# Performance work log

Measured on AMD Instinct MI355X. Metric: run time of the kernel, lower is better.

Reference implementation:

```python
import jax, jax.numpy as jnp
import numpy as np

B, S, V, D, H = 8, 256, 32000, 1024, 1024
NLAY_H, NLAY_L, HEADS = 2, 2, 8
RATIO, N_LOW, N_HIGH = 4, 16, 4
HD = H // HEADS


def setup_inputs():
    key = jax.random.key(0)
    ks = jax.random.split(key, 16)
    s = 0.02
    f = lambda k, shape: (jax.random.normal(k, shape) * s).astype(jnp.float32)
    return {
        "input_ids": jax.random.randint(ks[0], (B, S), 0, V),
        "emb": f(ks[1], (V, D)),
        "pos": f(ks[2], (S, D)),
        "Wih_h": f(ks[3], (NLAY_H, 3 * H, H)),
        "bih_h": jnp.zeros((NLAY_H, 3 * H), jnp.float32),
        "Whh_h": f(ks[4], (NLAY_H, 3 * H, H)),
        "bhh_h": jnp.zeros((NLAY_H, 3 * H), jnp.float32),
        "Win": f(ks[5], (H, 2 * H)),
        "bin_": jnp.zeros((H,), jnp.float32),
        "Wq": f(ks[6], (H, H)),
        "Wk": f(ks[7], (H, H)),
        "Wv": f(ks[8], (H, H)),
        "Wo": f(ks[9], (H, H)),
        "Wih_l": f(ks[10], (NLAY_L, 3 * H, H)),
        "bih_l": jnp.zeros((NLAY_L, 3 * H), jnp.float32),
        "Whh_l": f(ks[11], (NLAY_L, 3 * H, H)),
        "bhh_l": jnp.zeros((NLAY_L, 3 * H), jnp.float32),
        "ln_g": jnp.ones((H,), jnp.float32),
        "ln_b": jnp.zeros((H,), jnp.float32),
        "Wout": f(ks[12], (V, H)),
    }


def gru_cell(x, h, Wih, bih, Whh, bhh):
    gx = x @ Wih.T + bih  # [B, 3H]
    gh = h @ Whh.T + bhh
    xr, xz, xn = jnp.split(gx, 3, axis=-1)
    hr, hz, hn = jnp.split(gh, 3, axis=-1)
    r = jax.nn.sigmoid(xr + hr)
    z = jax.nn.sigmoid(xz + hz)
    n = jnp.tanh(xn + r * hn)
    return (1.0 - z) * n + z * h


def _forward(input_ids, emb, pos, Wih_h, bih_h, Whh_h, bhh_h, Win, bin_,
             Wq, Wk, Wv, Wo, Wih_l, bih_l, Whh_l, bhh_l, ln_g, ln_b, Wout):
    embeds = emb[input_ids] + pos[None, :S]  # [B, S, D]
    inv_sqrt_hd = np.float32(1.0 / np.sqrt(HD))

    def high_mod(x, hs):  # hs: [NLAY_H, B, H]
        new = []
        for l in range(NLAY_H):
            x = gru_cell(x, hs[l], Wih_h[l], bih_h[l], Whh_h[l], bhh_h[l])
            new.append(x)
        return jnp.stack(new), x

    def low_mod(x, high_cur, hist, mask, ls):
        # input projection over [embed ; current high state]
        inp = jax.nn.gelu(jnp.concatenate([x, high_cur], axis=-1) @ Win.T + bin_)  # [B, H]
        # multi-head cross-attention over high-state history (causal in high steps)
        q = (inp @ Wq.T).reshape(B, HEADS, HD)
        k = (hist @ Wk.T).reshape(B, N_HIGH, HEADS, HD)
        v = (hist @ Wv.T).reshape(B, N_HIGH, HEADS, HD)
        scores = jnp.einsum('bhd,bthd->bht', q, k) * inv_sqrt_hd
        scores = jnp.where(mask[None, None, :], scores, jnp.float32(-1e9))
        attn = jax.nn.softmax(scores, axis=-1)
        ctx = jnp.einsum('bht,bthd->bhd', attn, v).reshape(B, H) @ Wo.T
        x2 = inp + ctx
        new = []
        for l in range(NLAY_L):
            x2 = gru_cell(x2, ls[l], Wih_l[l], bih_l[l], Whh_l[l], bhh_l[l])
            new.append(x2)
        return jnp.stack(new), x2

    def step(carry, t):
        hs_all, ls_all, hist = carry
        e = embeds[:, t]  # [B, D]
        low_step = t % N_LOW
        high_step = low_step // RATIO
        do_high = (low_step % RATIO) == 0
        hs = hs_all[high_step]
        new_hs, high_out = high_mod(e, hs)
        hs_all = hs_all.at[high_step].set(jnp.where(do_high, new_hs, hs))
        hist = hist.at[:, high_step].set(jnp.where(do_high, high_out, hist[:, high_step]))
        mask = jnp.arange(N_HIGH) <= high_step
        ls = ls_all[low_step]
        new_ls, low_out = low_mod(e, hist[:, high_step], hist, mask, ls)
        ls_all = ls_all.at[low_step].set(new_ls)
        mu = low_out.mean(axis=-1, keepdims=True)
        var = ((low_out - mu) ** 2).mean(axis=-1, keepdims=True)
        y = (low_out - mu) / jnp.sqrt(var + 1e-5) * ln_g + ln_b
        return (hs_all, ls_all, hist), y @ Wout.T  # [B, V]

    hs0 = jnp.zeros((N_HIGH, NLAY_H, B, H), jnp.float32)
    ls0 = jnp.zeros((N_LOW, NLAY_L, B, H), jnp.float32)
    hist0 = jnp.zeros((B, N_HIGH, H), jnp.float32)
    _, logits = jax.lax.scan(step, (hs0, ls0, hist0), jnp.arange(S))
    return jnp.transpose(logits, (1, 0, 2))  # [B, S, V]


def reference(input_ids, emb, pos, Wih_h, bih_h, Whh_h, bhh_h, Win, bin_,
              Wq, Wk, Wv, Wo, Wih_l, bih_l, Whh_l, bhh_l, ln_g, ln_b, Wout):
    return _forward(input_ids, emb, pos, Wih_h, bih_h, Whh_h, bhh_h, Win, bin_,
                    Wq, Wk, Wv, Wo, Wih_l, bih_l, Whh_l, bhh_l, ln_g, ln_b, Wout)
```

## Files before the change

kernel.cpp:

```cpp
#include <hip/hip_runtime.h>

typedef unsigned short u16;
typedef float f32x4 __attribute__((ext_vector_type(4)));
typedef __bf16 bf16x8 __attribute__((ext_vector_type(8)));
typedef u16 u16x8 __attribute__((ext_vector_type(8)));

#define DEVFN __device__ __forceinline__


DEVFN u16 f2bf(float f) {
  unsigned u = __builtin_bit_cast(unsigned, f);
  unsigned r = u + 0x7FFFu + ((u >> 16) & 1u);
  return (u16)(r >> 16);
}

DEVFN bf16x8 cvt8(const float* p) {
  float4 f0 = *reinterpret_cast<const float4*>(p);
  float4 f1 = *reinterpret_cast<const float4*>(p + 4);
  u16x8 u;
  u[0] = f2bf(f0.x); u[1] = f2bf(f0.y); u[2] = f2bf(f0.z); u[3] = f2bf(f0.w);
  u[4] = f2bf(f1.x); u[5] = f2bf(f1.y); u[6] = f2bf(f1.z); u[7] = f2bf(f1.w);
  return __builtin_bit_cast(bf16x8, u);
}

DEVFN bf16x8 ldbf(const u16* p) { return *reinterpret_cast<const bf16x8*>(p); }
DEVFN float sigm(float x) { return 1.f / (1.f + expf(-x)); }

DEVFN void gload16(const u16* g, u16* l) {
  __builtin_amdgcn_global_load_lds(
      (const __attribute__((address_space(1))) void*)g,
      (__attribute__((address_space(3))) void*)l, 16, 0, 0);
}

template<int NTSTORE, int OUTF, int BF16OUT, int CADD>
__global__ __launch_bounds__(256) void gemm_lds(
    const u16* __restrict__ A, const u16* __restrict__ W,
    const float* __restrict__ Cadd,
    float* __restrict__ OUT, u16* __restrict__ OUTbf,
    int ldo, int mtiles) {
  __shared__ u16 smA[2][128 * 32];
  __shared__ u16 smB[2][128 * 32];

  int nwg = gridDim.x;
  int orig = blockIdx.x;
  int q = nwg >> 3, r = nwg & 7;
  int xcd = orig & 7, idx = orig >> 3;
  int wg = (xcd < r ? xcd * (q + 1) : r * (q + 1) + (xcd - r) * q) + idx;
  int m0 = (wg % mtiles) * 128;
  int n0 = (wg / mtiles) * 128;

  int tid = threadIdx.x;
  int wv = tid >> 6, lane = tid & 63;
  int lrow = lane >> 2;
  int gcol = ((lane & 3) ^ ((lrow >> 1) & 3)) << 3;

  const u16* gA = A + (size_t)(m0 + wv * 32 + lrow) * 1024 + gcol;
  const u16* gB = W + (size_t)(n0 + wv * 32 + lrow) * 1024 + gcol;
  u16* lA0 = &smA[0][(wv * 32) * 32];
  u16* lA1 = &smA[0][(wv * 32 + 16) * 32];
  u16* lB0 = &smB[0][(wv * 32) * 32];
  u16* lB1 = &smB[0][(wv * 32 + 16) * 32];
  const int BUFO = 128 * 32;

  f32x4 acc[4][4];
#pragma unroll
  for (int mi = 0; mi < 4; ++mi)
#pragma unroll
    for (int ni = 0; ni < 4; ++ni) acc[mi][ni] = f32x4{0.f, 0.f, 0.f, 0.f};

  int qm = (wv >> 1) * 64, qn = (wv & 1) * 64;
  int lr = lane & 15;
  int kk = (lane >> 4) << 3;

  int offA[4], offB[4];
#pragma unroll
  for (int i = 0; i < 4; ++i) {
    int ra = qm + i * 16 + lr;
    offA[i] = ra * 64 + ((kk ^ (((ra >> 1) & 3) << 3)) << 1);
    int rbw = qn + i * 16 + lr;
    offB[i] = rbw * 64 + ((kk ^ (((rbw >> 1) & 3) << 3)) << 1);
  }
  const char* baseA = (const char*)&smA[0][0];
  const char* baseB = (const char*)&smB[0][0];

  gload16(gA, lA0);
  gload16(gA + 16 * 1024, lA1);
  gload16(gB, lB0);
  gload16(gB + 16 * 1024, lB1);

  for (int kt = 0; kt < 32; ++kt) {
    int buf = kt & 1;
    __syncthreads();
    if (kt < 31) {
      int k0 = (kt + 1) << 5;
      int bo = (buf ^ 1) * BUFO;
      gload16(gA + k0, lA0 + bo);
      gload16(gA + 16 * 1024 + k0, lA1 + bo);
      gload16(gB + k0, lB0 + bo);
      gload16(gB + 16 * 1024 + k0, lB1 + bo);
    }
    int bb = buf * (BUFO * 2);
    bf16x8 av[4], bv[4];
#pragma unroll
    for (int i = 0; i < 4; ++i) {
      av[i] = *(const bf16x8*)(baseA + bb + offA[i]);
      bv[i] = *(const bf16x8*)(baseB + bb + offB[i]);
    }
#pragma unroll
    for (int mi = 0; mi < 4; ++mi)
#pragma unroll
      for (int ni = 0; ni < 4; ++ni)
        acc[mi][ni] = __builtin_amdgcn_mfma_f32_16x16x32_bf16(av[mi], bv[ni], acc[mi][ni], 0, 0, 0);
  }

  int rb = (lane >> 4) << 2;
#pragma unroll
  for (int mi = 0; mi < 4; ++mi)
#pragma unroll
    for (int ni = 0; ni < 4; ++ni)
#pragma unroll
      for (int rr = 0; rr < 4; ++rr) {
        int row = m0 + qm + mi * 16 + rb + rr;
        int col = n0 + qn + ni * 16 + lr;
        size_t o = (size_t)row * (size_t)ldo + col;
        float v = acc[mi][ni][rr];
        if constexpr (CADD) v += Cadd[o];
        if constexpr (OUTF) {
          if constexpr (NTSTORE) __builtin_nontemporal_store(v, &OUT[o]);
          else OUT[o] = v;
        }
        if constexpr (BF16OUT) OUTbf[o] = f2bf(v);
      }
}

template<int MT, int NT, int KW>
__global__ __launch_bounds__(64 * KW) void gemm2(
    const u16* __restrict__ A, int lda,
    const void* __restrict__ Wp, int ldw, int kwoff, int wbf,
    const float* __restrict__ Cadd, int ldc,
    float* __restrict__ OUT, u16* __restrict__ OUTbf, int ldo, int K) {
  int tid = threadIdx.x;
  int kw = tid >> 6;
  int lane = tid & 63;
  int lr = lane & 15;
  int kk = (lane >> 4) << 3;
  int n0 = blockIdx.x * (16 * NT);
  int m0 = blockIdx.y * (16 * MT);
  int KP = K / KW;
  int kb = kw * KP + kk;

  f32x4 acc[MT][NT];
#pragma unroll
  for (int mi = 0; mi < MT; ++mi)
#pragma unroll
    for (int ni = 0; ni < NT; ++ni) acc[mi][ni] = f32x4{0.f, 0.f, 0.f, 0.f};

  const u16* ap[MT];
#pragma unroll
  for (int mi = 0; mi < MT; ++mi) ap[mi] = A + (size_t)(m0 + mi * 16 + lr) * (size_t)lda + kb;

  if (wbf) {
    const u16* wb[NT];
#pragma unroll
    for (int ni = 0; ni < NT; ++ni)
      wb[ni] = (const u16*)Wp + (size_t)(n0 + ni * 16 + lr) * (size_t)ldw + kwoff + kb;
    for (int k0 = 0; k0 < KP; k0 += 32) {
      bf16x8 wv[NT];
#pragma unroll
      for (int ni = 0; ni < NT; ++ni) wv[ni] = ldbf(wb[ni] + k0);
#pragma unroll
      for (int mi = 0; mi < MT; ++mi) {
        bf16x8 a = ldbf(ap[mi] + k0);
#pragma unroll
        for (int ni = 0; ni < NT; ++ni)
          acc[mi][ni] = __builtin_amdgcn_mfma_f32_16x16x32_bf16(a, wv[ni], acc[mi][ni], 0, 0, 0);
      }
    }
  } else {
    const float* wf[NT];
#pragma unroll
    for (int ni = 0; ni < NT; ++ni)
      wf[ni] = (const float*)Wp + (size_t)(n0 + ni * 16 + lr) * (size_t)ldw + kwoff + kb;
    for (int k0 = 0; k0 < KP; k0 += 32) {
      bf16x8 wv[NT];
#pragma unroll
      for (int ni = 0; ni < NT; ++ni) wv[ni] = cvt8(wf[ni] + k0);
#pragma unroll
      for (int mi = 0; mi < MT; ++mi) {
        bf16x8 a = ldbf(ap[mi] + k0);
#pragma unroll
        for (int ni = 0; ni < NT; ++ni)
          acc[mi][ni] = __builtin_amdgcn_mfma_f32_16x16x32_bf16(a, wv[ni], acc[mi][ni], 0, 0, 0);
      }
    }
  }

  if constexpr (KW > 1) {
    __shared__ f32x4 red[KW][MT * NT][64];
#pragma unroll
    for (int mi = 0; mi < MT; ++mi)
#pragma unroll
      for (int ni = 0; ni < NT; ++ni) red[kw][mi * NT + ni][lane] = acc[mi][ni];
    __syncthreads();
    if (kw) return;
    for (int w2 = 1; w2 < KW; ++w2)
#pragma unroll
      for (int mi = 0; mi < MT; ++mi)
#pragma unroll
        for (int ni = 0; ni < NT; ++ni) acc[mi][ni] += red[w2][mi * NT + ni][lane];
  }

  int rb = (lane >> 4) << 2;
#pragma unroll
  for (int mi = 0; mi < MT; ++mi)
#pragma unroll
    for (int ni = 0; ni < NT; ++ni)
#pragma unroll
      for (int rr = 0; rr < 4; ++rr) {
        int row = m0 + mi * 16 + rb + rr;
        int col = n0 + ni * 16 + lr;
        size_t o = (size_t)row * (size_t)ldo + col;
        float v = acc[mi][ni][rr];
        if (Cadd) v += Cadd[(size_t)row * (size_t)ldc + col];
        if (OUT) OUT[o] = v;
        if (OUTbf) OUTbf[o] = f2bf(v);
      }
}

struct GruP {
  const u16* X; const u16* Hb; const float* Hf;
  const u16* Wbih; const u16* Wbhh;
  const float* Wfih; const float* Wfhh;
  const float* bih; const float* bhh;
  float* Hof; u16* Hob; u16* hist;
};

__global__ __launch_bounds__(256) void gru_dual(GruP pa, GruP pb, int tiles1, int wbf) {
  GruP p; int m0;
  if ((int)blockIdx.y < tiles1) { p = pa; m0 = blockIdx.y * 32; }
  else { p = pb; m0 = ((int)blockIdx.y - tiles1) * 32; }
  int tid = threadIdx.x;
  int kw = tid >> 6;
  int lane = tid & 63;
  int lr = lane & 15;
  int kk = (lane >> 4) << 3;
  int j0 = blockIdx.x * 16;
  const int KP = 256;
  int kb = kw * KP + kk;

  f32x4 aR[2], aZ[2], aNX[2], aNH[2];
#pragma unroll
  for (int mi = 0; mi < 2; ++mi) {
    aR[mi] = f32x4{0.f, 0.f, 0.f, 0.f};
    aZ[mi] = f32x4{0.f, 0.f, 0.f, 0.f};
    aNX[mi] = f32x4{0.f, 0.f, 0.f, 0.f};
    aNH[mi] = f32x4{0.f, 0.f, 0.f, 0.f};
  }

  const u16* xp[2];
  const u16* hp[2];
#pragma unroll
  for (int mi = 0; mi < 2; ++mi) {
    size_t ro = (size_t)(m0 + mi * 16 + lr) * 1024 + kb;
    xp[mi] = p.X + ro;
    hp[mi] = p.Hb + ro;
  }

  size_t wro = (size_t)(j0 + lr) * 1024 + kb;
  if (wbf) {
    const u16 *pxr = p.Wbih + wro, *pxz = p.Wbih + wro + 1048576, *pxn = p.Wbih + wro + 2097152;
    const u16 *phr = p.Wbhh + wro, *phz = p.Wbhh + wro + 1048576, *phn = p.Wbhh + wro + 2097152;
    for (int k0 = 0; k0 < KP; k0 += 32) {
      bf16x8 wxr = ldbf(pxr + k0), wxz = ldbf(pxz + k0), wxn = ldbf(pxn + k0);
      bf16x8 whr = ldbf(phr + k0), whz = ldbf(phz + k0), whn = ldbf(phn + k0);
#pragma unroll
      for (int mi = 0; mi < 2; ++mi) {
        bf16x8 ax = ldbf(xp[mi] + k0);
        bf16x8 ah = ldbf(hp[mi] + k0);
        aR[mi] = __builtin_amdgcn_mfma_f32_16x16x32_bf16(ax, wxr, aR[mi], 0, 0, 0);
        aR[mi] = __builtin_amdgcn_mfma_f32_16x16x32_bf16(ah, whr, aR[mi], 0, 0, 0);
        aZ[mi] = __builtin_amdgcn_mfma_f32_16x16x32_bf16(ax, wxz, aZ[mi], 0, 0, 0);
        aZ[mi] = __builtin_amdgcn_mfma_f32_16x16x32_bf16(ah, whz, aZ[mi], 0, 0, 0);
        aNX[mi] = __builtin_amdgcn_mfma_f32_16x16x32_bf16(ax, wxn, aNX[mi], 0, 0, 0);
        aNH[mi] = __builtin_amdgcn_mfma_f32_16x16x32_bf16(ah, whn, aNH[mi], 0, 0, 0);
      }
    }
  } else {
    const float *pxr = p.Wfih + wro, *pxz = p.Wfih + wro + 1048576, *pxn = p.Wfih + wro + 2097152;
    const float *phr = p.Wfhh + wro, *phz = p.Wfhh + wro + 1048576, *phn = p.Wfhh + wro + 2097152;
    for (int k0 = 0; k0 < KP; k0 += 32) {
      bf16x8 wxr = cvt8(pxr + k0), wxz = cvt8(pxz + k0), wxn = cvt8(pxn + k0);
      bf16x8 whr = cvt8(phr + k0), whz = cvt8(phz + k0), whn = cvt8(phn + k0);
#pragma unroll
      for (int mi = 0; mi < 2; ++mi) {
        bf16x8 ax = ldbf(xp[mi] + k0);
        bf16x8 ah = ldbf(hp[mi] + k0);
        aR[mi] = __builtin_amdgcn_mfma_f32_16x16x32_bf16(ax, wxr, aR[mi], 0, 0, 0);
        aR[mi] = __builtin_amdgcn_mfma_f32_16x16x32_bf16(ah, whr, aR[mi], 0, 0, 0);
        aZ[mi] = __builtin_amdgcn_mfma_f32_16x16x32_bf16(ax, wxz, aZ[mi], 0, 0, 0);
        aZ[mi] = __builtin_amdgcn_mfma_f32_16x16x32_bf16(ah, whz, aZ[mi], 0, 0, 0);
        aNX[mi] = __builtin_amdgcn_mfma_f32_16x16x32_bf16(ax, wxn, aNX[mi], 0, 0, 0);
        aNH[mi] = __builtin_amdgcn_mfma_f32_16x16x32_bf16(ah, whn, aNH[mi], 0, 0, 0);
      }
    }
  }

  {
    __shared__ f32x4 red[4][8][64];
#pragma unroll
    for (int mi = 0; mi < 2; ++mi) {
      red[kw][mi * 4 + 0][lane] = aR[mi];
      red[kw][mi * 4 + 1][lane] = aZ[mi];
      red[kw][mi * 4 + 2][lane] = aNX[mi];
      red[kw][mi * 4 + 3][lane] = aNH[mi];
    }
    __syncthreads();
    if (kw) return;
    for (int w2 = 1; w2 < 4; ++w2)
#pragma unroll
      for (int mi = 0; mi < 2; ++mi) {
        aR[mi] += red[w2][mi * 4 + 0][lane];
        aZ[mi] += red[w2][mi * 4 + 1][lane];
        aNX[mi] += red[w2][mi * 4 + 2][lane];
        aNH[mi] += red[w2][mi * 4 + 3][lane];
      }
  }

  int c = j0 + lr;
  float br = p.bih[c] + p.bhh[c];
  float bz = p.bih[1024 + c] + p.bhh[1024 + c];
  float bnx = p.bih[2048 + c];
  float bnh = p.bhh[2048 + c];
  int rb = (lane >> 4) << 2;
#pragma unroll
  for (int mi = 0; mi < 2; ++mi)
#pragma unroll
    for (int rr = 0; rr < 4; ++rr) {
      int row = m0 + mi * 16 + rb + rr;
      float r = sigm(aR[mi][rr] + br);
      float z = sigm(aZ[mi][rr] + bz);
      float n = tanhf(aNX[mi][rr] + bnx + r * (aNH[mi][rr] + bnh));
      size_t o = (size_t)row * 1024 + c;
      float hv = (1.f - z) * n + z * p.Hf[o];
      p.Hof[o] = hv;
      u16 hb = f2bf(hv);
      p.Hob[o] = hb;
      if (p.hist) p.hist[o] = hb;
    }
}

__global__ __launch_bounds__(256) void gemm_big(const u16* __restrict__ A,
                                                const void* __restrict__ Wp, int wbf,
                                                float* __restrict__ OUT) {
  int wv = threadIdx.x >> 6;
  int lane = threadIdx.x & 63;
  int lr = lane & 15;
  int kk = (lane >> 4) << 3;
  int m0 = blockIdx.x * 256 + wv * 64;
  int n0 = blockIdx.y * 64;

  f32x4 acc[4][4];
#pragma unroll
  for (int mi = 0; mi < 4; ++mi)
#pragma unroll
    for (int ni = 0; ni < 4; ++ni) acc[mi][ni] = f32x4{0.f, 0.f, 0.f, 0.f};

  const u16* ap[4];
#pragma unroll
  for (int mi = 0; mi < 4; ++mi) ap[mi] = A + (size_t)(m0 + mi * 16 + lr) * 1024 + kk;

  const float* wf[4];
#pragma unroll
  for (int ni = 0; ni < 4; ++ni) wf[ni] = (const float*)Wp + (size_t)(n0 + ni * 16 + lr) * 1024 + kk;
  for (int k0 = 0; k0 < 1024; k0 += 32) {
    bf16x8 wvv[4];
#pragma unroll
    for (int ni = 0; ni < 4; ++ni) wvv[ni] = cvt8(wf[ni] + k0);
#pragma unroll
    for (int mi = 0; mi < 4; ++mi) {
      bf16x8 a = ldbf(ap[mi] + k0);
#pragma unroll
      for (int ni = 0; ni < 4; ++ni)
        acc[mi][ni] = __builtin_amdgcn_mfma_f32_16x16x32_bf16(a, wvv[ni], acc[mi][ni], 0, 0, 0);
    }
  }

  int rb = (lane >> 4) << 2;
#pragma unroll
  for (int mi = 0; mi < 4; ++mi)
#pragma unroll
    for (int ni = 0; ni < 4; ++ni)
#pragma unroll
      for (int rr = 0; rr < 4; ++rr) {
        size_t o = (size_t)(m0 + mi * 16 + rb + rr) * 32000 + (size_t)(n0 + ni * 16 + lr);
        __builtin_nontemporal_store(acc[mi][ni][rr], &OUT[o]);
      }
}

struct CvtSeg { const float* src; u16* dst; int src_ld; int col_off; int log2c; int nblk; };
struct CvtArgs { CvtSeg seg[11]; int nseg; };

__global__ void cvt_all(CvtArgs a) {
  int blk = blockIdx.x;
  int s = 0;
  while (s < a.nseg - 1 && blk >= a.seg[s].nblk) { blk -= a.seg[s].nblk; ++s; }
  const CvtSeg g = a.seg[s];
  size_t idx = ((size_t)blk * 256 + threadIdx.x) * 8;
  size_t row = idx >> g.log2c;
  int col = (int)(idx & ((1u << g.log2c) - 1));
  const float* sp = g.src + row * (size_t)g.src_ld + g.col_off + col;
  *reinterpret_cast<u16x8*>(g.dst + idx) = __builtin_bit_cast(u16x8, cvt8(sp));
}

__global__ void embed_kernel(const int* __restrict__ ids, const float* __restrict__ emb,
                             const float* __restrict__ pos, u16* __restrict__ out) {
  int idx = blockIdx.x * 256 + threadIdx.x;
  int e8 = (idx & 127) << 3;
  int rb = idx >> 7;
  int t = rb >> 3, b = rb & 7;
  int w = t >> 4, lsp = t & 15, g = lsp >> 2, o = lsp & 3;
  int R = ((w << 4) + (o << 2) + g) * 8 + b;
  int tok = ids[b * 256 + t];
  const float* ep = emb + (size_t)tok * 1024 + e8;
  const float* pp = pos + (size_t)t * 1024 + e8;
  u16x8 u;
#pragma unroll
  for (int i = 0; i < 8; ++i) u[i] = f2bf(ep[i] + pp[i]);
  *reinterpret_cast<u16x8*>(out + (size_t)R * 1024 + e8) = u;
}

__global__ void inp_all(const float* __restrict__ einp, const float* __restrict__ kvhAll,
                        const float* __restrict__ bin, float* __restrict__ inpb,
                        u16* __restrict__ inpbf) {
  int idx = blockIdx.x * 256 + threadIdx.x;
  int r = idx >> 10, j = idx & 1023;
  int w = r >> 7, r7 = r & 127;
  int g = (r7 >> 3) & 3, b = r7 & 7;
  float x = einp[idx] + kvhAll[(size_t)(w * 32 + g * 8 + b) * 3072 + 2048 + j] + bin[j];
  float t = tanhf(0.7978845608028654f * (x + 0.044715f * x * x * x));
  float v = 0.5f * x * (1.f + t);
  inpb[idx] = v;
  inpbf[idx] = f2bf(v);
}

__global__ void attn_all(const float* __restrict__ qb, const float* __restrict__ kvhAll,
                         u16* __restrict__ ctxbf) {
  int r = blockIdx.x;
  int w = r >> 7, r7 = r & 127;
  int sp = r7 >> 3;
  int g = sp & 3;
  int b = r7 & 7;
  int lane = threadIdx.x;
  const float* kvb = kvhAll + (size_t)w * 32 * 3072;
  __shared__ float aw[8][4];
  if (lane < 32) {
    int head = lane >> 2, t = lane & 3;
    float s = 0.f;
    if (t <= g) {
      const float* qp = qb + (size_t)r * 1024 + head * 128;
      const float* kp = kvb + (size_t)(t * 8 + b) * 3072 + head * 128;
      for (int d = 0; d < 128; ++d) s += qp[d] * kp[d];
      s *= 0.08838834764831845f;
    }
    float sc[4];
    sc[0] = __shfl(s, (head << 2) + 0);
    sc[1] = __shfl(s, (head << 2) + 1);
    sc[2] = __shfl(s, (head << 2) + 2);
    sc[3] = __shfl(s, (head << 2) + 3);
    if (t == 0) {
      float mx = -1e30f;
      for (int u = 0; u <= g; ++u) mx = fmaxf(mx, sc[u]);
      float p[4] = {0.f, 0.f, 0.f, 0.f};
      float den = 0.f;
      for (int u = 0; u <= g; ++u) { p[u] = expf(sc[u] - mx); den += p[u]; }
      float inv = 1.f / den;
      for (int u = 0; u < 4; ++u) aw[head][u] = (u <= g) ? p[u] * inv : 0.f;
    }
  }
  __syncthreads();
  for (int idx = lane; idx < 1024; idx += 64) {
    int head = idx >> 7;
    float acc = 0.f;
#pragma unroll
    for (int t = 0; t < 4; ++t) acc += aw[head][t] * kvb[(size_t)(t * 8 + b) * 3072 + 1024 + idx];
    ctxbf[(size_t)r * 1024 + idx] = f2bf(acc);
  }
}

__global__ void ln_all(const float* __restrict__ ls1f, const float* __restrict__ g_,
                       const float* __restrict__ b_, u16* __restrict__ Ybf) {
  int bid = blockIdx.x;
  int w = bid >> 7, r7 = bid & 127;
  int tid = threadIdx.x;
  const float* x = ls1f + (size_t)(w + 1) * 131072 + (size_t)r7 * 1024;
  float s = 0.f, s2 = 0.f;
  for (int j = tid; j < 1024; j += 256) { float v = x[j]; s += v; s2 += v * v; }
  for (int off = 32; off; off >>= 1) { s += __shfl_xor(s, off); s2 += __shfl_xor(s2, off); }
  __shared__ float rs[4], rs2[4], mv[2];
  int wv = tid >> 6;
  if ((tid & 63) == 0) { rs[wv] = s; rs2[wv] = s2; }
  __syncthreads();
  if (tid == 0) {
    float S = rs[0] + rs[1] + rs[2] + rs[3];
    float S2 = rs2[0] + rs2[1] + rs2[2] + rs2[3];
    float mu = S * (1.f / 1024.f);
    float var = S2 * (1.f / 1024.f) - mu * mu;
    mv[0] = mu;
    mv[1] = rsqrtf(var + 1e-5f);
  }
  __syncthreads();
  float mu = mv[0], rstd = mv[1];
  int sp = r7 >> 3, b = r7 & 7;
  int g = sp & 3, o = sp >> 2;
  int t = w * 16 + g * 4 + o;
  u16* yrow = Ybf + (size_t)(b * 256 + t) * 1024;
  for (int j = tid; j < 1024; j += 256) {
    float v = (x[j] - mu) * rstd * g_[j] + b_[j];
    yrow[j] = f2bf(v);
  }
}

extern "C" void kernel_launch(void* const* d_in, const int* in_sizes, int n_in,
                              void* d_out, int out_size, void* d_ws, size_t ws_size,
                              hipStream_t stream) {
  const int* ids = (const int*)d_in[0];
  const float* emb = (const float*)d_in[1];
  const float* pos = (const float*)d_in[2];
  const float* Wih_h = (const float*)d_in[3];
  const float* bih_h = (const float*)d_in[4];
  const float* Whh_h = (const float*)d_in[5];
  const float* bhh_h = (const float*)d_in[6];
  const float* Win = (const float*)d_in[7];
  const float* bin_ = (const float*)d_in[8];
  const float* Wq = (const float*)d_in[9];
  const float* Wk = (const float*)d_in[10];
  const float* Wv = (const float*)d_in[11];
  const float* Wo = (const float*)d_in[12];
  const float* Wih_l = (const float*)d_in[13];
  const float* bih_l = (const float*)d_in[14];
  const float* Whh_l = (const float*)d_in[15];
  const float* bhh_l = (const float*)d_in[16];
  const float* ln_g = (const float*)d_in[17];
  const float* ln_b = (const float*)d_in[18];
  const float* Wout = (const float*)d_in[19];
  float* out = (float*)d_out;

  size_t off = 0;
  char* wsb = (char*)d_ws;
  auto allocF = [&](size_t n) { float* p = (float*)(wsb + off); off += n * 4; return p; };
  auto allocU = [&](size_t n) { u16* p = (u16*)(wsb + off); off += n * 2; return p; };

  float* hs0f = allocF((size_t)17 * 32768);
  float* hs1f = allocF((size_t)17 * 32768);
  float* ls0f = allocF((size_t)17 * 131072);
  float* ls1f = allocF((size_t)17 * 131072);
  u16* hs0b = allocU((size_t)17 * 32768);
  u16* hs1b = allocU((size_t)17 * 32768);
  u16* ls0b = allocU((size_t)17 * 131072);
  u16* ls1b = allocU((size_t)17 * 131072);
  u16* histAll = allocU(524288);
  u16* embB = allocU(2097152);
  float* einp = allocF(2097152);
  float* kvhAll = allocF((size_t)512 * 3072);
  float* inpb = allocF(2097152);
  u16* inpbf = allocU(2097152);
  float* qb = allocF(2097152);
  u16* ctxbf = allocU(2097152);
  u16* x2bf = allocU(2097152);
  u16* Ybf = allocU(2097152);

  const size_t WPACK_BYTES = (size_t)(4 * 6291456 + 1048576 + 1048576 + 1048576 + 3145728) * 2;
  bool packW = (off + WPACK_BYTES <= ws_size);
  u16 *WihHb = nullptr, *WhhHb = nullptr, *WihLb = nullptr, *WhhLb = nullptr;
  u16 *WinB0 = nullptr, *WqB = nullptr, *WoB = nullptr, *KVp = nullptr;
  if (packW) {
    WihHb = allocU(6291456);
    WhhHb = allocU(6291456);
    WihLb = allocU(6291456);
    WhhLb = allocU(6291456);
    WinB0 = allocU(1048576);
    WqB = allocU(1048576);
    WoB = allocU(1048576);
    KVp = allocU(3145728);
  }
  bool packWout = packW && (off + (size_t)32768000 * 2 <= ws_size);
  u16* WoutB = nullptr;
  if (packWout) WoutB = allocU(32768000);

  (void)hipMemsetAsync(hs0f, 0, 32768 * 4, stream);
  (void)hipMemsetAsync(hs1f, 0, 32768 * 4, stream);
  (void)hipMemsetAsync(ls0f, 0, 131072 * 4, stream);
  (void)hipMemsetAsync(ls1f, 0, 131072 * 4, stream);
  (void)hipMemsetAsync(hs0b, 0, 32768 * 2, stream);
  (void)hipMemsetAsync(hs1b, 0, 32768 * 2, stream);
  (void)hipMemsetAsync(ls0b, 0, 131072 * 2, stream);
  (void)hipMemsetAsync(ls1b, 0, 131072 * 2, stream);

  embed_kernel<<<1024, 256, 0, stream>>>(ids, emb, pos, embB);
  if (packW) {
    CvtArgs ca{};
    int ns = 0, tot = 0;
    auto add = [&](const float* s, u16* d, int ld, int co, int l2c, size_t nelem) {
      int nb = (int)(nelem / 2048);
      ca.seg[ns++] = CvtSeg{s, d, ld, co, l2c, nb};
      tot += nb;
    };
    add(Wih_h, WihHb, 1024, 0, 10, 6291456);
    add(Whh_h, WhhHb, 1024, 0, 10, 6291456);
    add(Wih_l, WihLb, 1024, 0, 10, 6291456);
    add(Whh_l, WhhLb, 1024, 0, 10, 6291456);
    add(Win, WinB0, 2048, 0, 10, 1048576);
    add(Wq, WqB, 1024, 0, 10, 1048576);
    add(Wo, WoB, 1024, 0, 10, 1048576);
    add(Wk, KVp, 1024, 0, 10, 1048576);
    add(Wv, KVp + 1048576, 1024, 0, 10, 1048576);
    add(Win, KVp + 2097152, 2048, 1024, 10, 1048576);
    if (packWout) add(Wout, WoutB, 1024, 0, 10, 32768000);
    ca.nseg = ns;
    cvt_all<<<tot, 256, 0, stream>>>(ca);
  }
  int wbfW = packW ? 1 : 0;

  if (packW)
    gemm_lds<0, 1, 0, 0><<<128, 256, 0, stream>>>(embB, WinB0, nullptr, einp, nullptr, 1024, 16);
  else
    gemm2<2, 2, 2><<<dim3(32, 64), 128, 0, stream>>>(
        embB, 1024, Win, 2048, 0, 0, nullptr, 0, einp, nullptr, 1024, 1024);

  const size_t LW = (size_t)3072 * 1024;
  auto HP = [&](int layer, int w) {
    GruP p;
    if (layer == 0) {
      p.X = embB + (size_t)w * 131072;
      p.Hb = hs0b + (size_t)w * 32768; p.Hf = hs0f + (size_t)w * 32768;
      p.Wbih = WihHb; p.Wbhh = WhhHb; p.Wfih = Wih_h; p.Wfhh = Whh_h;
      p.bih = bih_h; p.bhh = bhh_h;
      p.Hof = hs0f + (size_t)(w + 1) * 32768; p.Hob = hs0b + (size_t)(w + 1) * 32768;
      p.hist = nullptr;
    } else {
      p.X = hs0b + (size_t)(w + 1) * 32768;
      p.Hb = hs1b + (size_t)w * 32768; p.Hf = hs1f + (size_t)w * 32768;
      p.Wbih = WihHb ? WihHb + LW : nullptr; p.Wbhh = WhhHb ? WhhHb + LW : nullptr;
      p.Wfih = Wih_h + LW; p.Wfhh = Whh_h + LW;
      p.bih = bih_h + 3072; p.bhh = bhh_h + 3072;
      p.Hof = hs1f + (size_t)(w + 1) * 32768; p.Hob = hs1b + (size_t)(w + 1) * 32768;
      p.hist = histAll + (size_t)w * 32768;
    }
    return p;
  };
  auto LP = [&](int layer, int w) {
    GruP p;
    if (layer == 0) {
      p.X = x2bf + (size_t)w * 131072;
      p.Hb = ls0b + (size_t)w * 131072; p.Hf = ls0f + (size_t)w * 131072;
      p.Wbih = WihLb; p.Wbhh = WhhLb; p.Wfih = Wih_l; p.Wfhh = Whh_l;
      p.bih = bih_l; p.bhh = bhh_l;
      p.Hof = ls0f + (size_t)(w + 1) * 131072; p.Hob = ls0b + (size_t)(w + 1) * 131072;
      p.hist = nullptr;
    } else {
      p.X = ls0b + (size_t)(w + 1) * 131072;
      p.Hb = ls1b + (size_t)w * 131072; p.Hf = ls1f + (size_t)w * 131072;
      p.Wbih = WihLb ? WihLb + LW : nullptr; p.Wbhh = WhhLb ? WhhLb + LW : nullptr;
      p.Wfih = Wih_l + LW; p.Wfhh = Whh_l + LW;
      p.bih = bih_l + 3072; p.bhh = bhh_l + 3072;
      p.Hof = ls1f + (size_t)(w + 1) * 131072; p.Hob = ls1b + (size_t)(w + 1) * 131072;
      p.hist = nullptr;
    }
    return p;
  };

  gru_dual<<<dim3(64, 1), 256, 0, stream>>>(HP(0, 0), HP(0, 0), 1, wbfW);
  for (int d = 1; d <= 15; ++d)
    gru_dual<<<dim3(64, 2), 256, 0, stream>>>(HP(1, d - 1), HP(0, d), 1, wbfW);
  gru_dual<<<dim3(64, 1), 256, 0, stream>>>(HP(1, 15), HP(1, 15), 1, wbfW);

  if (packW) {
    gemm_lds<0, 1, 0, 0><<<96, 256, 0, stream>>>(histAll, KVp, nullptr, kvhAll, nullptr, 3072, 4);
  } else {
    gemm2<2, 2, 2><<<dim3(32, 16), 128, 0, stream>>>(
        histAll, 1024, Wk, 1024, 0, 0, nullptr, 0, kvhAll, nullptr, 3072, 1024);
    gemm2<2, 2, 2><<<dim3(32, 16), 128, 0, stream>>>(
        histAll, 1024, Wv, 1024, 0, 0, nullptr, 0, kvhAll + 1024, nullptr, 3072, 1024);
    gemm2<2, 2, 2><<<dim3(32, 16), 128, 0, stream>>>(
        histAll, 1024, Win, 2048, 1024, 0, nullptr, 0, kvhAll + 2048, nullptr, 3072, 1024);
  }
  inp_all<<<8192, 256, 0, stream>>>(einp, kvhAll, bin_, inpb, inpbf);
  if (packW)
    gemm_lds<0, 1, 0, 0><<<128, 256, 0, stream>>>(inpbf, WqB, nullptr, qb, nullptr, 1024, 16);
  else
    gemm2<2, 2, 2><<<dim3(32, 64), 128, 0, stream>>>(
        inpbf, 1024, Wq, 1024, 0, 0, nullptr, 0, qb, nullptr, 1024, 1024);
  attn_all<<<2048, 64, 0, stream>>>(qb, kvhAll, ctxbf);
  if (packW)
    gemm_lds<0, 0, 1, 1><<<128, 256, 0, stream>>>(ctxbf, WoB, inpb, nullptr, x2bf, 1024, 16);
  else
    gemm2<2, 2, 2><<<dim3(32, 64), 128, 0, stream>>>(
        ctxbf, 1024, Wo, 1024, 0, 0, inpb, 1024, nullptr, x2bf, 1024, 1024);

  gru_dual<<<dim3(64, 4), 256, 0, stream>>>(LP(0, 0), LP(0, 0), 4, wbfW);
  for (int d = 1; d <= 15; ++d)
    gru_dual<<<dim3(64, 8), 256, 0, stream>>>(LP(1, d - 1), LP(0, d), 4, wbfW);
  gru_dual<<<dim3(64, 4), 256, 0, stream>>>(LP(1, 15), LP(1, 15), 4, wbfW);

  ln_all<<<2048, 256, 0, stream>>>(ls1f, ln_g, ln_b, Ybf);
  if (packWout)
    gemm_lds<1, 1, 0, 0><<<4000, 256, 0, stream>>>(Ybf, WoutB, nullptr, out, nullptr, 32000, 16);
  else
    gemm_big<<<dim3(8, 500), 256, 0, stream>>>(Ybf, Wout, 0, out);
}
```

Before: 1.081 ms.

## Replace per-step GRU kernel launches with persistent cooperative grid-synced kernel

Replaces the 17 separate gru_dual launches for each wavefront-pipelined GRU chain (high and low modules) with a single cooperative kernel that loops over the diagonal steps and uses grid.sync between them. The goal is to remove kernel launch and inter-launch gaps on the sequential critical path. In exchange it adds grid-wide barrier costs, and idle blocks must still join every barrier. It falls back to the launch loop if the cooperative launch fails, and the GRU body is factored into a shared device function.

```diff
diff --git a/kernel.cpp b/kernel.cpp
--- a/kernel.cpp
+++ b/kernel.cpp
@@ -1,4 +1,7 @@
 #include <hip/hip_runtime.h>
+#include <hip/hip_cooperative_groups.h>
+
+namespace cg = cooperative_groups;
 
 typedef unsigned short u16;
 typedef float f32x4 __attribute__((ext_vector_type(4)));
@@ -227,6 +230,140 @@
       }
 }
 
+DEVFN void gru_step_body(const u16* __restrict__ X, const u16* __restrict__ Hb,
+                         const float* __restrict__ Hf,
+                         const u16* __restrict__ Wih, const u16* __restrict__ Whh,
+                         const float* __restrict__ bih, const float* __restrict__ bhh,
+                         float* __restrict__ Hof, u16* __restrict__ Hob,
+                         u16* __restrict__ hist,
+                         int m0, int j0, int kw, int lane,
+                         f32x4 (*red)[8][64]) {
+  int lr = lane & 15;
+  int kk = (lane >> 4) << 3;
+  const int KP = 256;
+  int kb = kw * KP + kk;
+
+  f32x4 aR[2], aZ[2], aNX[2], aNH[2];
+#pragma unroll
+  for (int mi = 0; mi < 2; ++mi) {
+    aR[mi] = f32x4{0.f, 0.f, 0.f, 0.f};
+    aZ[mi] = f32x4{0.f, 0.f, 0.f, 0.f};
+    aNX[mi] = f32x4{0.f, 0.f, 0.f, 0.f};
+    aNH[mi] = f32x4{0.f, 0.f, 0.f, 0.f};
+  }
+
+  const u16* xp[2];
+  const u16* hp[2];
+#pragma unroll
+  for (int mi = 0; mi < 2; ++mi) {
+    size_t ro = (size_t)(m0 + mi * 16 + lr) * 1024 + kb;
+    xp[mi] = X + ro;
+    hp[mi] = Hb + ro;
+  }
+
+  size_t wro = (size_t)(j0 + lr) * 1024 + kb;
+  const u16 *pxr = Wih + wro, *pxz = Wih + wro + 1048576, *pxn = Wih + wro + 2097152;
+  const u16 *phr = Whh + wro, *phz = Whh + wro + 1048576, *phn = Whh + wro + 2097152;
+  for (int k0 = 0; k0 < KP; k0 += 32) {
+    bf16x8 wxr = ldbf(pxr + k0), wxz = ldbf(pxz + k0), wxn = ldbf(pxn + k0);
+    bf16x8 whr = ldbf(phr + k0), whz = ldbf(phz + k0), whn = ldbf(phn + k0);
+#pragma unroll
+    for (int mi = 0; mi < 2; ++mi) {
+      bf16x8 ax = ldbf(xp[mi] + k0);
+      bf16x8 ah = ldbf(hp[mi] + k0);
+      aR[mi] = __builtin_amdgcn_mfma_f32_16x16x32_bf16(ax, wxr, aR[mi], 0, 0, 0);
+      aR[mi] = __builtin_amdgcn_mfma_f32_16x16x32_bf16(ah, whr, aR[mi], 0, 0, 0);
+      aZ[mi] = __builtin_amdgcn_mfma_f32_16x16x32_bf16(ax, wxz, aZ[mi], 0, 0, 0);
+      aZ[mi] = __builtin_amdgcn_mfma_f32_16x16x32_bf16(ah, whz, aZ[mi], 0, 0, 0);
+      aNX[mi] = __builtin_amdgcn_mfma_f32_16x16x32_bf16(ax, wxn, aNX[mi], 0, 0, 0);
+      aNH[mi] = __builtin_amdgcn_mfma_f32_16x16x32_bf16(ah, whn, aNH[mi], 0, 0, 0);
+    }
+  }
+
+#pragma unroll
+  for (int mi = 0; mi < 2; ++mi) {
+    red[kw][mi * 4 + 0][lane] = aR[mi];
+    red[kw][mi * 4 + 1][lane] = aZ[mi];
+    red[kw][mi * 4 + 2][lane] = aNX[mi];
+    red[kw][mi * 4 + 3][lane] = aNH[mi];
+  }
+  __syncthreads();
+  if (kw == 0) {
+    for (int w2 = 1; w2 < 4; ++w2)
+#pragma unroll
+      for (int mi = 0; mi < 2; ++mi) {
+        aR[mi] += red[w2][mi * 4 + 0][lane];
+        aZ[mi] += red[w2][mi * 4 + 1][lane];
+        aNX[mi] += red[w2][mi * 4 + 2][lane];
+        aNH[mi] += red[w2][mi * 4 + 3][lane];
+      }
+    int c = j0 + lr;
+    float br = bih[c] + bhh[c];
+    float bz = bih[1024 + c] + bhh[1024 + c];
+    float bnx = bih[2048 + c];
+    float bnh = bhh[2048 + c];
+    int rb = (lane >> 4) << 2;
+#pragma unroll
+    for (int mi = 0; mi < 2; ++mi)
+#pragma unroll
+      for (int rr = 0; rr < 4; ++rr) {
+        int row = m0 + mi * 16 + rb + rr;
+        float r = sigm(aR[mi][rr] + br);
+        float z = sigm(aZ[mi][rr] + bz);
+        float n = tanhf(aNX[mi][rr] + bnx + r * (aNH[mi][rr] + bnh));
+        size_t o = (size_t)row * 1024 + c;
+        float hv = (1.f - z) * n + z * Hf[o];
+        Hof[o] = hv;
+        u16 hb = f2bf(hv);
+        Hob[o] = hb;
+        if (hist) hist[o] = hb;
+      }
+  }
+}
+
+struct ChainArgs {
+  const u16* X0; size_t xstride;
+  float* h0f; u16* h0b;
+  float* h1f; u16* h1b;
+  size_t sstride;
+  const u16* Wih; const u16* Whh;
+  const float* bih; const float* bhh;
+  u16* hist;
+  int nm;
+};
+
+__global__ __launch_bounds__(256) void gru_chain(ChainArgs A) {
+  cg::grid_group grid = cg::this_grid();
+  __shared__ f32x4 red[4][8][64];
+  int tid = threadIdx.x;
+  int kw = tid >> 6, lane = tid & 63;
+  int j0 = blockIdx.x * 16;
+  int yy = blockIdx.y;
+  int probA = (yy < A.nm) ? 1 : 0;
+  int m0 = (probA ? yy : yy - A.nm) * 32;
+  const size_t LW = (size_t)3072 * 1024;
+
+  for (int d = 0; d <= 16; ++d) {
+    int active = probA ? (d >= 1) : (d <= 15);
+    if (active) {
+      int w = probA ? d - 1 : d;
+      int layer = probA;
+      const u16* X = probA ? (A.h0b + (size_t)(w + 1) * A.sstride)
+                           : (A.X0 + (size_t)w * A.xstride);
+      float* hf = layer ? A.h1f : A.h0f;
+      u16* hb = layer ? A.h1b : A.h0b;
+      gru_step_body(X, hb + (size_t)w * A.sstride, hf + (size_t)w * A.sstride,
+                    A.Wih + (size_t)layer * LW, A.Whh + (size_t)layer * LW,
+                    A.bih + layer * 3072, A.bhh + layer * 3072,
+                    hf + (size_t)(w + 1) * A.sstride, hb + (size_t)(w + 1) * A.sstride,
+                    (probA && A.hist) ? (A.hist + (size_t)w * 32768) : nullptr,
+                    m0, j0, kw, lane, red);
+    }
+    __threadfence();
+    grid.sync();
+  }
+}
+
 struct GruP {
   const u16* X; const u16* Hb; const float* Hf;
   const u16* Wbih; const u16* Wbhh;
@@ -247,6 +384,13 @@
   int j0 = blockIdx.x * 16;
   const int KP = 256;
   int kb = kw * KP + kk;
+  __shared__ f32x4 red[4][8][64];
+
+  if (wbf) {
+    gru_step_body(p.X, p.Hb, p.Hf, p.Wbih, p.Wbhh, p.bih, p.bhh,
+                  p.Hof, p.Hob, p.hist, m0, j0, kw, lane, red);
+    return;
+  }
 
   f32x4 aR[2], aZ[2], aNX[2], aNH[2];
 #pragma unroll
@@ -256,7 +400,6 @@
     aNX[mi] = f32x4{0.f, 0.f, 0.f, 0.f};
     aNH[mi] = f32x4{0.f, 0.f, 0.f, 0.f};
   }
-
   const u16* xp[2];
   const u16* hp[2];
 #pragma unroll
@@ -265,67 +408,41 @@
     xp[mi] = p.X + ro;
     hp[mi] = p.Hb + ro;
   }
-
   size_t wro = (size_t)(j0 + lr) * 1024 + kb;
-  if (wbf) {
-    const u16 *pxr = p.Wbih + wro, *pxz = p.Wbih + wro + 1048576, *pxn = p.Wbih + wro + 2097152;
-    const u16 *phr = p.Wbhh + wro, *phz = p.Wbhh + wro + 1048576, *phn = p.Wbhh + wro + 2097152;
-    for (int k0 = 0; k0 < KP; k0 += 32) {
-      bf16x8 wxr = ldbf(pxr + k0), wxz = ldbf(pxz + k0), wxn = ldbf(pxn + k0);
-      bf16x8 whr = ldbf(phr + k0), whz = ldbf(phz + k0), whn = ldbf(phn + k0);
-#pragma unroll
-      for (int mi = 0; mi < 2; ++mi) {
-        bf16x8 ax = ldbf(xp[mi] + k0);
-        bf16x8 ah = ldbf(hp[mi] + k0);
-        aR[mi] = __builtin_amdgcn_mfma_f32_16x16x32_bf16(ax, wxr, aR[mi], 0, 0, 0);
-        aR[mi] = __builtin_amdgcn_mfma_f32_16x16x32_bf16(ah, whr, aR[mi], 0, 0, 0);
-        aZ[mi] = __builtin_amdgcn_mfma_f32_16x16x32_bf16(ax, wxz, aZ[mi], 0, 0, 0);
-        aZ[mi] = __builtin_amdgcn_mfma_f32_16x16x32_bf16(ah, whz, aZ[mi], 0, 0, 0);
-        aNX[mi] = __builtin_amdgcn_mfma_f32_16x16x32_bf16(ax, wxn, aNX[mi], 0, 0, 0);
-        aNH[mi] = __builtin_amdgcn_mfma_f32_16x16x32_bf16(ah, whn, aNH[mi], 0, 0, 0);
-      }
-    }
-  } else {
-    const float *pxr = p.Wfih + wro, *pxz = p.Wfih + wro + 1048576, *pxn = p.Wfih + wro + 2097152;
-    const float *phr = p.Wfhh + wro, *phz = p.Wfhh + wro + 1048576, *phn = p.Wfhh + wro + 2097152;
-    for (int k0 = 0; k0 < KP; k0 += 32) {
-      bf16x8 wxr = cvt8(pxr + k0), wxz = cvt8(pxz + k0), wxn = cvt8(pxn + k0);
-      bf16x8 whr = cvt8(phr + k0), whz = cvt8(phz + k0), whn = cvt8(phn + k0);
-#pragma unroll
-      for (int mi = 0; mi < 2; ++mi) {
-        bf16x8 ax = ldbf(xp[mi] + k0);
-        bf16x8 ah = ldbf(hp[mi] + k0);
-        aR[mi] = __builtin_amdgcn_mfma_f32_16x16x32_bf16(ax, wxr, aR[mi], 0, 0, 0);
-        aR[mi] = __builtin_amdgcn_mfma_f32_16x16x32_bf16(ah, whr, aR[mi], 0, 0, 0);
-        aZ[mi] = __builtin_amdgcn_mfma_f32_16x16x32_bf16(ax, wxz, aZ[mi], 0, 0, 0);
-        aZ[mi] = __builtin_amdgcn_mfma_f32_16x16x32_bf16(ah, whz, aZ[mi], 0, 0, 0);
-        aNX[mi] = __builtin_amdgcn_mfma_f32_16x16x32_bf16(ax, wxn, aNX[mi], 0, 0, 0);
-        aNH[mi] = __builtin_amdgcn_mfma_f32_16x16x32_bf16(ah, whn, aNH[mi], 0, 0, 0);
-      }
-    }
-  }
-
-  {
-    __shared__ f32x4 red[4][8][64];
+  const float *pxr = p.Wfih + wro, *pxz = p.Wfih + wro + 1048576, *pxn = p.Wfih + wro + 2097152;
+  const float *phr = p.Wfhh + wro, *phz = p.Wfhh + wro + 1048576, *phn = p.Wfhh + wro + 2097152;
+  for (int k0 = 0; k0 < KP; k0 += 32) {
+    bf16x8 wxr = cvt8(pxr + k0), wxz = cvt8(pxz + k0), wxn = cvt8(pxn + k0);
+    bf16x8 whr = cvt8(phr + k0), whz = cvt8(phz + k0), whn = cvt8(phn + k0);
 #pragma unroll
     for (int mi = 0; mi < 2; ++mi) {
-      red[kw][mi * 4 + 0][lane] = aR[mi];
-      red[kw][mi * 4 + 1][lane] = aZ[mi];
-      red[kw][mi * 4 + 2][lane] = aNX[mi];
-      red[kw][mi * 4 + 3][lane] = aNH[mi];
-    }
-    __syncthreads();
-    if (kw) return;
-    for (int w2 = 1; w2 < 4; ++w2)
-#pragma unroll
-      for (int mi = 0; mi < 2; ++mi) {
-        aR[mi] += red[w2][mi * 4 + 0][lane];
-        aZ[mi] += red[w2][mi * 4 + 1][lane];
-        aNX[mi] += red[w2][mi * 4 + 2][lane];
-        aNH[mi] += red[w2][mi * 4 + 3][lane];
-      }
-  }
-
+      bf16x8 ax = ldbf(xp[mi] + k0);
+      bf16x8 ah = ldbf(hp[mi] + k0);
+      aR[mi] = __builtin_amdgcn_mfma_f32_16x16x32_bf16(ax, wxr, aR[mi], 0, 0, 0);
+      aR[mi] = __builtin_amdgcn_mfma_f32_16x16x32_bf16(ah, whr, aR[mi], 0, 0, 0);
+      aZ[mi] = __builtin_amdgcn_mfma_f32_16x16x32_bf16(ax, wxz, aZ[mi], 0, 0, 0);
+      aZ[mi] = __builtin_amdgcn_mfma_f32_16x16x32_bf16(ah, whz, aZ[mi], 0, 0, 0);
+      aNX[mi] = __builtin_amdgcn_mfma_f32_16x16x32_bf16(ax, wxn, aNX[mi], 0, 0, 0);
+      aNH[mi] = __builtin_amdgcn_mfma_f32_16x16x32_bf16(ah, whn, aNH[mi], 0, 0, 0);
+    }
+  }
+#pragma unroll
+  for (int mi = 0; mi < 2; ++mi) {
+    red[kw][mi * 4 + 0][lane] = aR[mi];
+    red[kw][mi * 4 + 1][lane] = aZ[mi];
+    red[kw][mi * 4 + 2][lane] = aNX[mi];
+    red[kw][mi * 4 + 3][lane] = aNH[mi];
+  }
+  __syncthreads();
+  if (kw) return;
+  for (int w2 = 1; w2 < 4; ++w2)
+#pragma unroll
+    for (int mi = 0; mi < 2; ++mi) {
+      aR[mi] += red[w2][mi * 4 + 0][lane];
+      aZ[mi] += red[w2][mi * 4 + 1][lane];
+      aNX[mi] += red[w2][mi * 4 + 2][lane];
+      aNH[mi] += red[w2][mi * 4 + 3][lane];
+    }
   int c = j0 + lr;
   float br = p.bih[c] + p.bhh[c];
   float bz = p.bih[1024 + c] + p.bhh[1024 + c];
@@ -668,11 +785,33 @@
     }
     return p;
   };
-
-  gru_dual<<<dim3(64, 1), 256, 0, stream>>>(HP(0, 0), HP(0, 0), 1, wbfW);
-  for (int d = 1; d <= 15; ++d)
-    gru_dual<<<dim3(64, 2), 256, 0, stream>>>(HP(1, d - 1), HP(0, d), 1, wbfW);
-  gru_dual<<<dim3(64, 1), 256, 0, stream>>>(HP(1, 15), HP(1, 15), 1, wbfW);
+  auto high_loop = [&]() {
+    gru_dual<<<dim3(64, 1), 256, 0, stream>>>(HP(0, 0), HP(0, 0), 1, wbfW);
+    for (int d = 1; d <= 15; ++d)
+      gru_dual<<<dim3(64, 2), 256, 0, stream>>>(HP(1, d - 1), HP(0, d), 1, wbfW);
+    gru_dual<<<dim3(64, 1), 256, 0, stream>>>(HP(1, 15), HP(1, 15), 1, wbfW);
+  };
+  auto low_loop = [&]() {
+    gru_dual<<<dim3(64, 4), 256, 0, stream>>>(LP(0, 0), LP(0, 0), 4, wbfW);
+    for (int d = 1; d <= 15; ++d)
+      gru_dual<<<dim3(64, 8), 256, 0, stream>>>(LP(1, d - 1), LP(0, d), 4, wbfW);
+    gru_dual<<<dim3(64, 4), 256, 0, stream>>>(LP(1, 15), LP(1, 15), 4, wbfW);
+  };
+
+  if (packW) {
+    ChainArgs ha;
+    ha.X0 = embB; ha.xstride = 131072;
+    ha.h0f = hs0f; ha.h0b = hs0b; ha.h1f = hs1f; ha.h1b = hs1b;
+    ha.sstride = 32768;
+    ha.Wih = WihHb; ha.Whh = WhhHb; ha.bih = bih_h; ha.bhh = bhh_h;
+    ha.hist = histAll; ha.nm = 1;
+    void* hargs[] = { &ha };
+    hipError_t e = hipLaunchCooperativeKernel((const void*)gru_chain, dim3(64, 2),
+                                              dim3(256), hargs, 0, stream);
+    if (e != hipSuccess) high_loop();
+  } else {
+    high_loop();
+  }
 
   if (packW) {
     gemm_lds<0, 1, 0, 0><<<96, 256, 0, stream>>>(histAll, KVp, nullptr, kvhAll, nullptr, 3072, 4);
@@ -697,10 +836,20 @@
     gemm2<2, 2, 2><<<dim3(32, 64), 128, 0, stream>>>(
         ctxbf, 1024, Wo, 1024, 0, 0, inpb, 1024, nullptr, x2bf, 1024, 1024);
 
-  gru_dual<<<dim3(64, 4), 256, 0, stream>>>(LP(0, 0), LP(0, 0), 4, wbfW);
-  for (int d = 1; d <= 15; ++d)
-    gru_dual<<<dim3(64, 8), 256, 0, stream>>>(LP(1, d - 1), LP(0, d), 4, wbfW);
-  gru_dual<<<dim3(64, 4), 256, 0, stream>>>(LP(1, 15), LP(1, 15), 4, wbfW);
+  if (packW) {
+    ChainArgs la;
+    la.X0 = x2bf; la.xstride = 131072;
+    la.h0f = ls0f; la.h0b = ls0b; la.h1f = ls1f; la.h1b = ls1b;
+    la.sstride = 131072;
+    la.Wih = WihLb; la.Whh = WhhLb; la.bih = bih_l; la.bhh = bhh_l;
+    la.hist = nullptr; la.nm = 4;
+    void* largs[] = { &la };
+    hipError_t e = hipLaunchCooperativeKernel((const void*)gru_chain, dim3(64, 8),
+                                              dim3(256), largs, 0, stream);
+    if (e != hipSuccess) low_loop();
+  } else {
+    low_loop();
+  }
 
   ln_all<<<2048, 256, 0, stream>>>(ls1f, ln_g, ln_b, Ybf);
   if (packWout)
```

Measured after the change: 3.327 ms. +207.8%, slower.
